# Kernel tuning notes

Measured on AMD Instinct MI355X. Metric: run time of the kernel, lower is better.

The kernel has to match this reference:

```python
import jax, jax.numpy as jnp
import numpy as np

BS, N, F, G, H, L, HFC, C, E = 8, 15135, 64, 73, 256, 3, 512, 2, 242160

def setup_inputs() -> dict:
    key = jax.random.key(0)
    ks = jax.random.split(key, 16)
    s = 0.02
    return {
        "x": jax.random.normal(ks[0], (BS, N, F), jnp.float32),
        "batch": jnp.zeros((BS,), jnp.int64),
        "edge_index": jax.random.randint(ks[1], (2, E), 0, N, jnp.int64),
        "nodes_graphlets": jax.random.uniform(ks[2], (N, G), jnp.float32),
        "W1": jax.random.normal(ks[3], (F + G, H), jnp.float32) * s,
        "b1": jnp.zeros((H,), jnp.float32),
        "W2": jax.random.normal(ks[4], (H, H), jnp.float32) * s,
        "b2": jnp.zeros((H,), jnp.float32),
        "W3": jax.random.normal(ks[5], (H, H), jnp.float32) * s,
        "b3": jnp.zeros((H,), jnp.float32),
        "fc_W": jax.random.normal(ks[6], (L * H, 1), jnp.float32) * s,
        "fc_b": jnp.zeros((1,), jnp.float32),
        "lin1_W": jax.random.normal(ks[7], (N, HFC), jnp.float32) * s,
        "lin1_b": jnp.zeros((HFC,), jnp.float32),
        "lin2_W": jax.random.normal(ks[8], (HFC, C), jnp.float32) * s,
        "lin2_b": jnp.zeros((C,), jnp.float32),
    }


def reference(x, batch, edge_index, nodes_graphlets, W1, b1, W2, b2, W3, b3,
              fc_W, fc_b, lin1_W, lin1_b, lin2_W, lin2_b):
    bs, n, _ = x.shape
    row, col = edge_index[0], edge_index[1]
    # GCN normalization with self-loops (edge_weight = 1): D^-1/2 (A+I) D^-1/2
    deg = jnp.zeros((n,), x.dtype).at[col].add(1.0) + 1.0
    dis = jax.lax.rsqrt(deg)
    norm = dis[row] * dis[col]          # [E]
    deg_inv = 1.0 / deg                 # self-loop coefficient dis[i]^2

    def gcn_conv(h, W, b):
        hw = h @ W                                  # [bs, n, H]
        msg = hw[:, row, :] * norm[None, :, None]   # gather src, scale
        agg = jnp.zeros_like(hw).at[:, col, :].add(msg)
        agg = agg + hw * deg_inv[None, :, None]     # self loops
        return agg + b

    # graphlet_mode == 'input': concat graphlet features to node features
    pe = jnp.broadcast_to(nodes_graphlets[None], (bs,) + nodes_graphlets.shape)
    h = jnp.concatenate([x, pe], axis=2)            # [bs, n, F+G]

    h1 = jax.nn.elu(gcn_conv(h, W1, b1))
    h2 = jax.nn.elu(gcn_conv(h1, W2, b2))
    h3 = jax.nn.elu(gcn_conv(h2, W3, b3))

    # mode == 'cat': stack along new last dim then flatten (torch stack+view order)
    hc = jnp.stack([h1, h2, h3], axis=-1).reshape(bs, n, -1)  # [bs, n, H*L]
    g = (hc @ fc_W + fc_b).reshape(bs, n)                     # [bs, n_genes]

    z = jax.nn.elu(g @ lin1_W + lin1_b)   # dropout: eval mode -> identity
    out = z @ lin2_W + lin2_b
    return jax.nn.log_softmax(out, axis=-1)
```

## Files before the change

kernel.cpp:

```cpp
#include <hip/hip_runtime.h>
#include <hip/hip_bf16.h>

using bf16 = __hip_bfloat16;
typedef short s16x8 __attribute__((ext_vector_type(8)));
typedef short s16x4 __attribute__((ext_vector_type(4)));
typedef float f32x4 __attribute__((ext_vector_type(4)));
typedef float f32x2 __attribute__((ext_vector_type(2)));

#define BSZ   8
#define NN    15135
#define FF    64
#define GG    73
#define HH    256
#define EE    242160
#define K1P   160
#define MREAL (BSZ * NN)
#define MPAD  (946 * 128)
#define HFC   512
#define NCHUNK 64
#define NCHUNKS ((NN + NCHUNK - 1) / NCHUNK)
#define SCANB  ((NN + 255) / 256)
#define FP8_INV_SCALE 0.015625f

#define GLOAD_LDS16(gp, lp)                                                     \
    __builtin_amdgcn_global_load_lds(                                           \
        (const __attribute__((address_space(1))) void*)(gp),                    \
        (__attribute__((address_space(3))) void*)(lp), 16, 0, 0)

__device__ __forceinline__ int colmap(int p) {
    return (p & 192) | ((p & 3) << 4) | ((p >> 2) & 15);
}

__global__ void k_deg(const int* __restrict__ col, int* __restrict__ cnt, int e) {
    int i = blockIdx.x * blockDim.x + threadIdx.x;
    if (i < e) atomicAdd(&cnt[col[i]], 1);
}

__global__ __launch_bounds__(256)
void k_scanA(const int* __restrict__ cnt, int* __restrict__ cursor,
             int* __restrict__ bsum) {
    __shared__ int ws[4];
    int i = blockIdx.x * 256 + threadIdx.x;
    int tid = threadIdx.x, lane = tid & 63, wid = tid >> 6;
    int v = (i < NN) ? cnt[i] : 0;
    int s = v;
    #pragma unroll
    for (int off = 1; off < 64; off <<= 1) {
        int t = __shfl_up(s, off);
        if (lane >= off) s += t;
    }
    if (lane == 63) ws[wid] = s;
    __syncthreads();
    int pre = 0;
    #pragma unroll
    for (int w = 0; w < 4; ++w) pre += (w < wid) ? ws[w] : 0;
    int incl = pre + s;
    if (i < NN) cursor[i] = incl;
    if (tid == 255) bsum[blockIdx.x] = incl;
}

__global__ __launch_bounds__(64)
void k_scanB(int* __restrict__ bsum, int* __restrict__ offs) {
    int t = threadIdx.x;
    int v = (t < SCANB) ? bsum[t] : 0;
    int s = v;
    #pragma unroll
    for (int off = 1; off < 64; off <<= 1) {
        int x = __shfl_up(s, off);
        if (t >= off) s += x;
    }
    if (t < SCANB) bsum[t] = s - v;
    if (t == 63) offs[NN] = s;
}

__global__ __launch_bounds__(256)
void k_scanC(const int* __restrict__ cnt, int* __restrict__ cursor,
             const int* __restrict__ bsum, int* __restrict__ offs,
             float* __restrict__ dis, float* __restrict__ dinv) {
    int i = blockIdx.x * 256 + threadIdx.x;
    if (i >= NN) return;
    int v = cnt[i];
    int excl = cursor[i] - v + bsum[blockIdx.x];
    offs[i] = excl;
    cursor[i] = excl;
    float d = (float)(v + 1);
    dis[i]  = rsqrtf(d);
    dinv[i] = (1.0f / d) * FP8_INV_SCALE;
}

__global__ void k_csr(const int* __restrict__ row, const int* __restrict__ col,
                      int* __restrict__ cursor, const float* __restrict__ dis,
                      int2* __restrict__ cpack, int e) {
    int i = blockIdx.x * blockDim.x + threadIdx.x;
    if (i >= e) return;
    int r = row[i], c = col[i];
    int p = atomicAdd(&cursor[c], 1);
    cpack[p] = make_int2(r, __float_as_int(dis[r] * dis[c] * FP8_INV_SCALE));
}

__global__ void k_prep_h0(const float* __restrict__ x, const float* __restrict__ gl,
                          bf16* __restrict__ h0) {
    int idx = blockIdx.x * blockDim.x + threadIdx.x;
    if (idx >= MREAL * (K1P / 8)) return;
    int m = idx / (K1P / 8);
    int q = idx - m * (K1P / 8);
    int j0 = q * 8;
    int n = m % NN;
    s16x8 o;
    #pragma unroll
    for (int k = 0; k < 8; ++k) {
        int j = j0 + k;
        float val;
        if (j < FF) val = x[(size_t)m * FF + j];
        else if (j < FF + GG) val = gl[(size_t)n * GG + (j - FF)];
        else val = 0.f;
        o[k] = (short)__bfloat16_as_ushort(__float2bfloat16(val));
    }
    *(s16x8*)&h0[(size_t)m * K1P + j0] = o;
}

__global__ void k_prep_w3(const float* __restrict__ W1, const float* __restrict__ W2,
                          const float* __restrict__ W3, bf16* __restrict__ W1T,
                          bf16* __restrict__ W2T, bf16* __restrict__ W3T) {
    int idx = blockIdx.x * blockDim.x + threadIdx.x;
    if (idx < 256 * K1P) {
        int nn = idx / K1P, kk = idx - nn * K1P;
        W1T[idx] = __float2bfloat16(
            kk < FF + GG ? 64.f * W1[(size_t)kk * 256 + nn] : 0.f);
    } else if (idx < 256 * K1P + 65536) {
        int j = idx - 256 * K1P;
        int nn = j >> 8, kk = j & 255;
        W2T[j] = __float2bfloat16(64.f * W2[(size_t)colmap(kk) * 256 + nn]);
    } else if (idx < 256 * K1P + 2 * 65536) {
        int j = idx - 256 * K1P - 65536;
        int nn = j >> 8, kk = j & 255;
        W3T[j] = __float2bfloat16(64.f * W3[(size_t)colmap(kk) * 256 + nn]);
    }
}

#define BK 32
template <int K>
__global__ __launch_bounds__(256)
void k_gemm(const bf16* __restrict__ A, const bf16* __restrict__ BT,
            unsigned char* __restrict__ C) {
    __shared__ __align__(16) short As[64 * BK];
    __shared__ __align__(16) short Bs[256 * BK];
    const int tid  = threadIdx.x;
    const int bm   = blockIdx.x * 64;
    const int lane = tid & 63, wave = tid >> 6;
    const int wn   = wave * 64;
    const int fr   = lane & 15, quad = lane >> 4;
    const int r    = tid >> 2;
    const int c    = (tid & 3) * 8;

    const bf16* Ap = A  + (size_t)(bm + r) * K + c;
    const bf16* Bp = BT + (size_t)r * K + c;
    short* AsT = As + tid * 8;
    short* BsT = Bs + tid * 8;

    f32x4 acc[4][4] = {};

    for (int k0 = 0; k0 < K; k0 += BK) {
        GLOAD_LDS16(Ap + k0, AsT);
        #pragma unroll
        for (int q = 0; q < 4; ++q)
            GLOAD_LDS16(Bp + (size_t)(q * 64) * K + k0, BsT + q * 64 * BK);
        __syncthreads();
        s16x8 af[4], bfv[4];
        #pragma unroll
        for (int i = 0; i < 4; ++i)
            af[i] = *(const s16x8*)&As[(i * 16 + fr) * BK + quad * 8];
        #pragma unroll
        for (int j = 0; j < 4; ++j)
            bfv[j] = *(const s16x8*)&Bs[(wn + j * 16 + fr) * BK + quad * 8];
        #pragma unroll
        for (int i = 0; i < 4; ++i)
            #pragma unroll
            for (int j = 0; j < 4; ++j)
                acc[i][j] = __builtin_amdgcn_mfma_f32_16x16x32_bf16(
                    af[i], bfv[j], acc[i][j], 0, 0, 0);
        __syncthreads();
    }

    #pragma unroll
    for (int i = 0; i < 4; ++i) {
        int rbase = bm + i * 16 + quad * 4;
        #pragma unroll
        for (int rr = 0; rr < 4; ++rr) {
            int row = rbase + rr;
            if (row >= MREAL) continue;
            unsigned wpack = (unsigned)__builtin_amdgcn_cvt_pk_fp8_f32(
                acc[i][0][rr], acc[i][1][rr], 0, false);
            wpack = (unsigned)__builtin_amdgcn_cvt_pk_fp8_f32(
                acc[i][2][rr], acc[i][3][rr], (int)wpack, true);
            *(unsigned*)&C[(size_t)row * 256 + wn + fr * 4] = wpack;
        }
    }
}

#define AGG_GRP 512
#define AGG_STRIDE (AGG_GRP * 4)
__global__ __launch_bounds__(256)
void k_agg(const unsigned char* __restrict__ hw, bf16* __restrict__ hout,
           const int* __restrict__ offs, const int2* __restrict__ cpack,
           const float* __restrict__ dinv,
           const float* __restrict__ bias, const float* __restrict__ fcW,
           float* __restrict__ g, int writeH) {
    const int b    = blockIdx.x & 7;
    const int grp  = blockIdx.x >> 3;
    const int wid  = threadIdx.x >> 6;
    const int lane = threadIdx.x & 63;
    const int wv   = grp * 4 + wid;
    const unsigned c4 = lane * 4;

    const unsigned char* hwb = hw + (size_t)b * NN * 256;

    float bias4[4], fw4[4];
    #pragma unroll
    for (int k = 0; k < 4; ++k) {
        int cl = colmap((int)c4 + k);
        bias4[k] = bias[cl];
        fw4[k]   = fcW[3 * cl];
    }

    for (int v0 = wv; v0 < NN; v0 += AGG_STRIDE) {
        const int v   = __builtin_amdgcn_readfirstlane(v0);
        const int beg = __builtin_amdgcn_readfirstlane(offs[v]);
        const int end = __builtin_amdgcn_readfirstlane(offs[v + 1]);
        const float di = dinv[v];
        f32x2 a01, a23;
        {
            unsigned q = *(const unsigned*)(hwb + (((unsigned)v) << 8) + c4);
            f32x2 t0 = __builtin_amdgcn_cvt_pk_f32_fp8(q, false);
            f32x2 t1 = __builtin_amdgcn_cvt_pk_f32_fp8(q, true);
            f32x2 dd = {di, di};
            a01 = dd * t0;
            a23 = dd * t1;
        }

        #define EDGE1(qv, mv) {                                            \
            f32x2 t0 = __builtin_amdgcn_cvt_pk_f32_fp8((qv), false);       \
            f32x2 t1 = __builtin_amdgcn_cvt_pk_f32_fp8((qv), true);        \
            f32x2 mm = {(mv), (mv)};                                       \
            a01 += mm * t0;                                                \
            a23 += mm * t1; }

        int e = beg;
        while (e + 8 <= end) {
            int2 ep[8];
            #pragma unroll
            for (int u = 0; u < 8; ++u) ep[u] = cpack[e + u];
            unsigned q[8];
            #pragma unroll
            for (int u = 0; u < 8; ++u)
                q[u] = *(const unsigned*)(hwb + (((unsigned)ep[u].x) << 8) + c4);
            #pragma unroll
            for (int u = 0; u < 8; ++u) EDGE1(q[u], __int_as_float(ep[u].y));
            e += 8;
        }
        if (e + 4 <= end) {
            int2 ep[4];
            #pragma unroll
            for (int u = 0; u < 4; ++u) ep[u] = cpack[e + u];
            unsigned q[4];
            #pragma unroll
            for (int u = 0; u < 4; ++u)
                q[u] = *(const unsigned*)(hwb + (((unsigned)ep[u].x) << 8) + c4);
            #pragma unroll
            for (int u = 0; u < 4; ++u) EDGE1(q[u], __int_as_float(ep[u].y));
            e += 4;
        }
        if (e + 2 <= end) {
            int2 ep0 = cpack[e], ep1 = cpack[e + 1];
            unsigned q0 = *(const unsigned*)(hwb + (((unsigned)ep0.x) << 8) + c4);
            unsigned q1 = *(const unsigned*)(hwb + (((unsigned)ep1.x) << 8) + c4);
            EDGE1(q0, __int_as_float(ep0.y));
            EDGE1(q1, __int_as_float(ep1.y));
            e += 2;
        }
        if (e < end) {
            int2 ep0 = cpack[e];
            unsigned q0 = *(const unsigned*)(hwb + (((unsigned)ep0.x) << 8) + c4);
            EDGE1(q0, __int_as_float(ep0.y));
        }
        #undef EDGE1

        float acc4[4] = {a01[0], a01[1], a23[0], a23[1]};
        float p = 0.f;
        s16x4 o4;
        #pragma unroll
        for (int k = 0; k < 4; ++k) {
            float hv = acc4[k] + bias4[k];
            hv = hv > 0.f ? hv : (__expf(hv) - 1.0f);
            o4[k] = (short)__bfloat16_as_ushort(__float2bfloat16(hv));
            p += hv * fw4[k];
        }
        if (writeH)
            *(s16x4*)&hout[((size_t)b * NN + v) * 256 + c4] = o4;

        #pragma unroll
        for (int off = 32; off; off >>= 1) p += __shfl_xor(p, off);
        if (lane == 0) g[(size_t)b * NN + v] += p;
    }
}

__global__ __launch_bounds__(256)
void k_lin1(const float* __restrict__ g, const float* __restrict__ fcb,
            const float* __restrict__ W, float* __restrict__ zpart) {
    const int ny = blockIdx.x;
    const int n0 = ny * NCHUNK;
    const int cnt = min(NCHUNK, NN - n0);
    const int tid = threadIdx.x;
    __shared__ float sg[8][NCHUNK];
    float fb = fcb[0];
    for (int idx = tid; idx < 8 * NCHUNK; idx += 256) {
        int b = idx / NCHUNK, nn = idx - b * NCHUNK;
        sg[b][nn] = (nn < cnt) ? (g[(size_t)b * NN + n0 + nn] + fb) : 0.f;
    }
    __syncthreads();
    float2 acc[8] = {};
    for (int nn = 0; nn < cnt; ++nn) {
        float2 w = *(const float2*)&W[(size_t)(n0 + nn) * HFC + tid * 2];
        #pragma unroll
        for (int b = 0; b < 8; ++b) {
            float gv = sg[b][nn];
            acc[b].x += gv * w.x;
            acc[b].y += gv * w.y;
        }
    }
    #pragma unroll
    for (int b = 0; b < 8; ++b)
        *(float2*)&zpart[(size_t)ny * 4096 + b * 512 + tid * 2] = acc[b];
}

__global__ __launch_bounds__(256)
void k_lin1red(const float* __restrict__ zpart, float* __restrict__ zacc) {
    int t = blockIdx.x * 256 + threadIdx.x;
    float s = 0.f;
    for (int c = 0; c < NCHUNKS; ++c) s += zpart[(size_t)c * 4096 + t];
    zacc[t] = s;
}

__global__ __launch_bounds__(512)
void k_final(const float* __restrict__ zacc, const float* __restrict__ l1b,
             const float* __restrict__ W2, const float* __restrict__ l2b,
             float* __restrict__ out) {
    __shared__ float r0[512], r1[512];
    int t = threadIdx.x;
    for (int b = 0; b < 8; ++b) {
        float zv = zacc[b * HFC + t] + l1b[t];
        zv = zv > 0.f ? zv : (__expf(zv) - 1.0f);
        r0[t] = zv * W2[t * 2 + 0];
        r1[t] = zv * W2[t * 2 + 1];
        __syncthreads();
        for (int s = 256; s; s >>= 1) {
            if (t < s) { r0[t] += r0[t + s]; r1[t] += r1[t + s]; }
            __syncthreads();
        }
        if (t == 0) {
            float o0 = r0[0] + l2b[0], o1 = r1[0] + l2b[1];
            float m = fmaxf(o0, o1);
            float lse = m + logf(expf(o0 - m) + expf(o1 - m));
            out[b * 2 + 0] = o0 - lse;
            out[b * 2 + 1] = o1 - lse;
        }
        __syncthreads();
    }
}

extern "C" void kernel_launch(void* const* d_in, const int* in_sizes, int n_in,
                              void* d_out, int out_size, void* d_ws, size_t ws_size,
                              hipStream_t stream) {
    const float* x    = (const float*)d_in[0];
    const int*   eidx = (const int*)d_in[2];
    const float* gl   = (const float*)d_in[3];
    const float* W1   = (const float*)d_in[4];
    const float* b1   = (const float*)d_in[5];
    const float* W2   = (const float*)d_in[6];
    const float* b2   = (const float*)d_in[7];
    const float* W3   = (const float*)d_in[8];
    const float* b3   = (const float*)d_in[9];
    const float* fcW  = (const float*)d_in[10];
    const float* fcb  = (const float*)d_in[11];
    const float* l1W  = (const float*)d_in[12];
    const float* l1b  = (const float*)d_in[13];
    const float* l2W  = (const float*)d_in[14];
    const float* l2b  = (const float*)d_in[15];
    float* out = (float*)d_out;

    size_t off = 0;
    auto alloc = [&](size_t bytes) {
        void* p = (char*)d_ws + off;
        off += (bytes + 255) & ~(size_t)255;
        return p;
    };
    bf16* bufA          = (bf16*)alloc((size_t)MPAD * 256 * 2);
    unsigned char* bufC = (unsigned char*)alloc((size_t)MPAD * 256);
    bf16* W1T      = (bf16*)alloc(256 * K1P * 2);
    bf16* W2T      = (bf16*)alloc(256 * 256 * 2);
    bf16* W3T      = (bf16*)alloc(256 * 256 * 2);
    int*  deg_cnt  = (int*)alloc(NN * 4);
    int*  offs     = (int*)alloc((NN + 1) * 4);
    int*  cursor   = (int*)alloc(NN * 4);
    int*  bsum     = (int*)alloc(SCANB * 4);
    float* dis     = (float*)alloc(NN * 4);
    float* dinv    = (float*)alloc(NN * 4);
    int2* cpack    = (int2*)alloc((size_t)EE * 8);
    float* g       = (float*)alloc((size_t)BSZ * NN * 4);

    float* zpart = (float*)bufC;
    float* zacc  = (float*)(bufC + (8 << 20));

    hipMemsetAsync(deg_cnt, 0, NN * 4, stream);
    hipMemsetAsync(g, 0, (size_t)BSZ * NN * 4, stream);

    const int* erow = eidx;
    const int* ecol = eidx + EE;

    k_deg<<<(EE + 255) / 256, 256, 0, stream>>>(ecol, deg_cnt, EE);
    k_scanA<<<SCANB, 256, 0, stream>>>(deg_cnt, cursor, bsum);
    k_scanB<<<1, 64, 0, stream>>>(bsum, offs);
    k_scanC<<<SCANB, 256, 0, stream>>>(deg_cnt, cursor, bsum, offs, dis, dinv);
    k_csr<<<(EE + 255) / 256, 256, 0, stream>>>(erow, ecol, cursor, dis,
                                                cpack, EE);

    k_prep_h0<<<(MREAL * (K1P / 8) + 255) / 256, 256, 0, stream>>>(x, gl, bufA);
    k_prep_w3<<<(256 * K1P + 2 * 65536 + 255) / 256, 256, 0, stream>>>(
        W1, W2, W3, W1T, W2T, W3T);

    dim3 ggrid(MPAD / 64);
    dim3 agrid(8 * AGG_GRP);

    k_gemm<K1P><<<ggrid, 256, 0, stream>>>(bufA, W1T, bufC);
    k_agg<<<agrid, 256, 0, stream>>>(bufC, bufA, offs, cpack, dinv,
                                     b1, fcW + 0, g, 1);
    k_gemm<256><<<ggrid, 256, 0, stream>>>(bufA, W2T, bufC);
    k_agg<<<agrid, 256, 0, stream>>>(bufC, bufA, offs, cpack, dinv,
                                     b2, fcW + 1, g, 1);
    k_gemm<256><<<ggrid, 256, 0, stream>>>(bufA, W3T, bufC);
    k_agg<<<agrid, 256, 0, stream>>>(bufC, bufA, offs, cpack, dinv,
                                     b3, fcW + 2, g, 0);

    k_lin1<<<NCHUNKS, 256, 0, stream>>>(g, fcb, l1W, zpart);
    k_lin1red<<<16, 256, 0, stream>>>(zpart, zacc);
    k_final<<<1, 512, 0, stream>>>(zacc, l1b, l2W, l2b, out);
}
```

Baseline: 459.8 us.

## Fuse setup kernels with grid barrier, merge prep and final reductions

Merges the degree count, three scan stages and CSR build into one persistent kernel synchronised by an atomic grid barrier. It also folds both memsets and the weight/h0 prep into a single prep kernel, and combines the lin1 reduction with the final layer into a per-batch kernel. The aggregation edge loop is unrolled to 16 edges for more loads in flight. This cuts launch count and serial tiny kernels, at the cost of relying on all 240 blocks being co-resident for the spin barrier and higher register pressure in the aggregation kernel.

```diff
diff --git a/kernel.cpp b/kernel.cpp
--- a/kernel.cpp
+++ b/kernel.cpp
@@ -31,110 +31,141 @@
     return (p & 192) | ((p & 3) << 4) | ((p >> 2) & 15);
 }
 
-__global__ void k_deg(const int* __restrict__ col, int* __restrict__ cnt, int e) {
-    int i = blockIdx.x * blockDim.x + threadIdx.x;
-    if (i < e) atomicAdd(&cnt[col[i]], 1);
-}
-
-__global__ __launch_bounds__(256)
-void k_scanA(const int* __restrict__ cnt, int* __restrict__ cursor,
-             int* __restrict__ bsum) {
-    __shared__ int ws[4];
-    int i = blockIdx.x * 256 + threadIdx.x;
-    int tid = threadIdx.x, lane = tid & 63, wid = tid >> 6;
-    int v = (i < NN) ? cnt[i] : 0;
-    int s = v;
-    #pragma unroll
-    for (int off = 1; off < 64; off <<= 1) {
-        int t = __shfl_up(s, off);
-        if (lane >= off) s += t;
-    }
-    if (lane == 63) ws[wid] = s;
-    __syncthreads();
-    int pre = 0;
-    #pragma unroll
-    for (int w = 0; w < 4; ++w) pre += (w < wid) ? ws[w] : 0;
-    int incl = pre + s;
-    if (i < NN) cursor[i] = incl;
-    if (tid == 255) bsum[blockIdx.x] = incl;
-}
-
-__global__ __launch_bounds__(64)
-void k_scanB(int* __restrict__ bsum, int* __restrict__ offs) {
-    int t = threadIdx.x;
-    int v = (t < SCANB) ? bsum[t] : 0;
-    int s = v;
-    #pragma unroll
-    for (int off = 1; off < 64; off <<= 1) {
-        int x = __shfl_up(s, off);
-        if (t >= off) s += x;
-    }
-    if (t < SCANB) bsum[t] = s - v;
-    if (t == 63) offs[NN] = s;
-}
-
-__global__ __launch_bounds__(256)
-void k_scanC(const int* __restrict__ cnt, int* __restrict__ cursor,
-             const int* __restrict__ bsum, int* __restrict__ offs,
-             float* __restrict__ dis, float* __restrict__ dinv) {
-    int i = blockIdx.x * 256 + threadIdx.x;
-    if (i >= NN) return;
-    int v = cnt[i];
-    int excl = cursor[i] - v + bsum[blockIdx.x];
-    offs[i] = excl;
-    cursor[i] = excl;
-    float d = (float)(v + 1);
-    dis[i]  = rsqrtf(d);
-    dinv[i] = (1.0f / d) * FP8_INV_SCALE;
-}
-
-__global__ void k_csr(const int* __restrict__ row, const int* __restrict__ col,
-                      int* __restrict__ cursor, const float* __restrict__ dis,
-                      int2* __restrict__ cpack, int e) {
-    int i = blockIdx.x * blockDim.x + threadIdx.x;
-    if (i >= e) return;
-    int r = row[i], c = col[i];
-    int p = atomicAdd(&cursor[c], 1);
-    cpack[p] = make_int2(r, __float_as_int(dis[r] * dis[c] * FP8_INV_SCALE));
-}
-
-__global__ void k_prep_h0(const float* __restrict__ x, const float* __restrict__ gl,
-                          bf16* __restrict__ h0) {
+#define PREP_H0_CNT (MREAL * (K1P / 8))
+#define PREP_W1_CNT (256 * K1P)
+#define PREP_W23_CNT 65536
+#define PREP_TOT (PREP_H0_CNT + PREP_W1_CNT + 2 * PREP_W23_CNT + NN + MREAL + 64)
+__global__ void k_prep(const float* __restrict__ x, const float* __restrict__ gl,
+                       bf16* __restrict__ h0,
+                       const float* __restrict__ W1, const float* __restrict__ W2,
+                       const float* __restrict__ W3, bf16* __restrict__ W1T,
+                       bf16* __restrict__ W2T, bf16* __restrict__ W3T,
+                       int* __restrict__ cnt, float* __restrict__ g,
+                       int* __restrict__ sync) {
     int idx = blockIdx.x * blockDim.x + threadIdx.x;
-    if (idx >= MREAL * (K1P / 8)) return;
-    int m = idx / (K1P / 8);
-    int q = idx - m * (K1P / 8);
-    int j0 = q * 8;
-    int n = m % NN;
-    s16x8 o;
-    #pragma unroll
-    for (int k = 0; k < 8; ++k) {
-        int j = j0 + k;
-        float val;
-        if (j < FF) val = x[(size_t)m * FF + j];
-        else if (j < FF + GG) val = gl[(size_t)n * GG + (j - FF)];
-        else val = 0.f;
-        o[k] = (short)__bfloat16_as_ushort(__float2bfloat16(val));
-    }
-    *(s16x8*)&h0[(size_t)m * K1P + j0] = o;
-}
-
-__global__ void k_prep_w3(const float* __restrict__ W1, const float* __restrict__ W2,
-                          const float* __restrict__ W3, bf16* __restrict__ W1T,
-                          bf16* __restrict__ W2T, bf16* __restrict__ W3T) {
-    int idx = blockIdx.x * blockDim.x + threadIdx.x;
-    if (idx < 256 * K1P) {
+    if (idx < PREP_H0_CNT) {
+        int m = idx / (K1P / 8);
+        int q = idx - m * (K1P / 8);
+        int j0 = q * 8;
+        int n = m % NN;
+        s16x8 o;
+        #pragma unroll
+        for (int k = 0; k < 8; ++k) {
+            int j = j0 + k;
+            float val;
+            if (j < FF) val = x[(size_t)m * FF + j];
+            else if (j < FF + GG) val = gl[(size_t)n * GG + (j - FF)];
+            else val = 0.f;
+            o[k] = (short)__bfloat16_as_ushort(__float2bfloat16(val));
+        }
+        *(s16x8*)&h0[(size_t)m * K1P + j0] = o;
+        return;
+    }
+    idx -= PREP_H0_CNT;
+    if (idx < PREP_W1_CNT) {
         int nn = idx / K1P, kk = idx - nn * K1P;
         W1T[idx] = __float2bfloat16(
             kk < FF + GG ? 64.f * W1[(size_t)kk * 256 + nn] : 0.f);
-    } else if (idx < 256 * K1P + 65536) {
-        int j = idx - 256 * K1P;
-        int nn = j >> 8, kk = j & 255;
-        W2T[j] = __float2bfloat16(64.f * W2[(size_t)colmap(kk) * 256 + nn]);
-    } else if (idx < 256 * K1P + 2 * 65536) {
-        int j = idx - 256 * K1P - 65536;
-        int nn = j >> 8, kk = j & 255;
-        W3T[j] = __float2bfloat16(64.f * W3[(size_t)colmap(kk) * 256 + nn]);
+        return;
+    }
+    idx -= PREP_W1_CNT;
+    if (idx < PREP_W23_CNT) {
+        int nn = idx >> 8, kk = idx & 255;
+        W2T[idx] = __float2bfloat16(64.f * W2[(size_t)colmap(kk) * 256 + nn]);
+        return;
+    }
+    idx -= PREP_W23_CNT;
+    if (idx < PREP_W23_CNT) {
+        int nn = idx >> 8, kk = idx & 255;
+        W3T[idx] = __float2bfloat16(64.f * W3[(size_t)colmap(kk) * 256 + nn]);
+        return;
+    }
+    idx -= PREP_W23_CNT;
+    if (idx < NN) { cnt[idx] = 0; return; }
+    idx -= NN;
+    if (idx < MREAL) { g[idx] = 0.f; return; }
+    idx -= MREAL;
+    if (idx < 64) sync[idx] = 0;
+}
+
+#define NB_SETUP 240
+__device__ __forceinline__ void gbar(int* sync, int target) {
+    __syncthreads();
+    if (threadIdx.x == 0) {
+        __threadfence();
+        atomicAdd(sync, 1);
+        while (atomicAdd(sync, 0) < target) __builtin_amdgcn_s_sleep(8);
+        __threadfence();
+    }
+    __syncthreads();
+}
+
+__global__ __launch_bounds__(256)
+void k_setup(const int* __restrict__ erow, const int* __restrict__ ecol,
+             int* __restrict__ cnt, int* __restrict__ offs,
+             int* __restrict__ cursor, int* __restrict__ bsum,
+             float* __restrict__ dis, float* __restrict__ dinv,
+             int2* __restrict__ cpack, int* __restrict__ sync) {
+    __shared__ int ws[4];
+    const int tid = threadIdx.x, bid = blockIdx.x;
+    const int gsz = NB_SETUP * 256;
+    const int gid = bid * 256 + tid;
+
+    for (int i = gid; i < EE; i += gsz) atomicAdd(&cnt[ecol[i]], 1);
+    gbar(sync, NB_SETUP);
+
+    if (bid < SCANB) {
+        int i = bid * 256 + tid;
+        int lane = tid & 63, wid = tid >> 6;
+        int v = (i < NN) ? cnt[i] : 0;
+        int s = v;
+        #pragma unroll
+        for (int off = 1; off < 64; off <<= 1) {
+            int t = __shfl_up(s, off);
+            if (lane >= off) s += t;
+        }
+        if (lane == 63) ws[wid] = s;
+        __syncthreads();
+        int pre = 0;
+        #pragma unroll
+        for (int w = 0; w < 4; ++w) pre += (w < wid) ? ws[w] : 0;
+        int incl = pre + s;
+        if (i < NN) cursor[i] = incl;
+        if (tid == 255) bsum[bid] = incl;
+    }
+    gbar(sync, 2 * NB_SETUP);
+
+    if (bid == 0 && tid < 64) {
+        int v = (tid < SCANB) ? bsum[tid] : 0;
+        int s = v;
+        #pragma unroll
+        for (int off = 1; off < 64; off <<= 1) {
+            int xx = __shfl_up(s, off);
+            if (tid >= off) s += xx;
+        }
+        if (tid < SCANB) bsum[tid] = s - v;
+        if (tid == 63) offs[NN] = s;
+    }
+    gbar(sync, 3 * NB_SETUP);
+
+    if (bid < SCANB) {
+        int i = bid * 256 + tid;
+        if (i < NN) {
+            int v = cnt[i];
+            int excl = cursor[i] - v + bsum[bid];
+            offs[i] = excl;
+            cursor[i] = excl;
+            float d = (float)(v + 1);
+            dis[i]  = rsqrtf(d);
+            dinv[i] = (1.0f / d) * FP8_INV_SCALE;
+        }
+    }
+    gbar(sync, 4 * NB_SETUP);
+
+    for (int i = gid; i < EE; i += gsz) {
+        int r = erow[i], c = ecol[i];
+        int p = atomicAdd(&cursor[c], 1);
+        cpack[p] = make_int2(r, __float_as_int(dis[r] * dis[c] * FP8_INV_SCALE));
     }
 }
 
@@ -246,7 +277,19 @@
             a23 += mm * t1; }
 
         int e = beg;
-        while (e + 8 <= end) {
+        while (e + 16 <= end) {
+            int2 ep[16];
+            #pragma unroll
+            for (int u = 0; u < 16; ++u) ep[u] = cpack[e + u];
+            unsigned q[16];
+            #pragma unroll
+            for (int u = 0; u < 16; ++u)
+                q[u] = *(const unsigned*)(hwb + (((unsigned)ep[u].x) << 8) + c4);
+            #pragma unroll
+            for (int u = 0; u < 16; ++u) EDGE1(q[u], __int_as_float(ep[u].y));
+            e += 16;
+        }
+        if (e + 8 <= end) {
             int2 ep[8];
             #pragma unroll
             for (int u = 0; u < 8; ++u) ep[u] = cpack[e + u];
@@ -333,38 +376,29 @@
         *(float2*)&zpart[(size_t)ny * 4096 + b * 512 + tid * 2] = acc[b];
 }
 
-__global__ __launch_bounds__(256)
-void k_lin1red(const float* __restrict__ zpart, float* __restrict__ zacc) {
-    int t = blockIdx.x * 256 + threadIdx.x;
+__global__ __launch_bounds__(512)
+void k_lin2(const float* __restrict__ zpart, const float* __restrict__ l1b,
+            const float* __restrict__ W2, const float* __restrict__ l2b,
+            float* __restrict__ out) {
+    __shared__ float r0[512], r1[512];
+    const int b = blockIdx.x, t = threadIdx.x;
     float s = 0.f;
-    for (int c = 0; c < NCHUNKS; ++c) s += zpart[(size_t)c * 4096 + t];
-    zacc[t] = s;
-}
-
-__global__ __launch_bounds__(512)
-void k_final(const float* __restrict__ zacc, const float* __restrict__ l1b,
-             const float* __restrict__ W2, const float* __restrict__ l2b,
-             float* __restrict__ out) {
-    __shared__ float r0[512], r1[512];
-    int t = threadIdx.x;
-    for (int b = 0; b < 8; ++b) {
-        float zv = zacc[b * HFC + t] + l1b[t];
-        zv = zv > 0.f ? zv : (__expf(zv) - 1.0f);
-        r0[t] = zv * W2[t * 2 + 0];
-        r1[t] = zv * W2[t * 2 + 1];
+    for (int c = 0; c < NCHUNKS; ++c) s += zpart[(size_t)c * 4096 + b * 512 + t];
+    float zv = s + l1b[t];
+    zv = zv > 0.f ? zv : (__expf(zv) - 1.0f);
+    r0[t] = zv * W2[t * 2 + 0];
+    r1[t] = zv * W2[t * 2 + 1];
+    __syncthreads();
+    for (int st = 256; st; st >>= 1) {
+        if (t < st) { r0[t] += r0[t + st]; r1[t] += r1[t + st]; }
         __syncthreads();
-        for (int s = 256; s; s >>= 1) {
-            if (t < s) { r0[t] += r0[t + s]; r1[t] += r1[t + s]; }
-            __syncthreads();
-        }
-        if (t == 0) {
-            float o0 = r0[0] + l2b[0], o1 = r1[0] + l2b[1];
-            float m = fmaxf(o0, o1);
-            float lse = m + logf(expf(o0 - m) + expf(o1 - m));
-            out[b * 2 + 0] = o0 - lse;
-            out[b * 2 + 1] = o1 - lse;
-        }
-        __syncthreads();
+    }
+    if (t == 0) {
+        float o0 = r0[0] + l2b[0], o1 = r1[0] + l2b[1];
+        float m = fmaxf(o0, o1);
+        float lse = m + logf(expf(o0 - m) + expf(o1 - m));
+        out[b * 2 + 0] = o0 - lse;
+        out[b * 2 + 1] = o1 - lse;
     }
 }
 
@@ -407,26 +441,18 @@
     float* dinv    = (float*)alloc(NN * 4);
     int2* cpack    = (int2*)alloc((size_t)EE * 8);
     float* g       = (float*)alloc((size_t)BSZ * NN * 4);
+    int*  sync     = (int*)alloc(64 * 4);
 
     float* zpart = (float*)bufC;
-    float* zacc  = (float*)(bufC + (8 << 20));
-
-    hipMemsetAsync(deg_cnt, 0, NN * 4, stream);
-    hipMemsetAsync(g, 0, (size_t)BSZ * NN * 4, stream);
 
     const int* erow = eidx;
     const int* ecol = eidx + EE;
 
-    k_deg<<<(EE + 255) / 256, 256, 0, stream>>>(ecol, deg_cnt, EE);
-    k_scanA<<<SCANB, 256, 0, stream>>>(deg_cnt, cursor, bsum);
-    k_scanB<<<1, 64, 0, stream>>>(bsum, offs);
-    k_scanC<<<SCANB, 256, 0, stream>>>(deg_cnt, cursor, bsum, offs, dis, dinv);
-    k_csr<<<(EE + 255) / 256, 256, 0, stream>>>(erow, ecol, cursor, dis,
-                                                cpack, EE);
-
-    k_prep_h0<<<(MREAL * (K1P / 8) + 255) / 256, 256, 0, stream>>>(x, gl, bufA);
-    k_prep_w3<<<(256 * K1P + 2 * 65536 + 255) / 256, 256, 0, stream>>>(
-        W1, W2, W3, W1T, W2T, W3T);
+    k_prep<<<(PREP_TOT + 255) / 256, 256, 0, stream>>>(
+        x, gl, bufA, W1, W2, W3, W1T, W2T, W3T, deg_cnt, g, sync);
+
+    k_setup<<<NB_SETUP, 256, 0, stream>>>(erow, ecol, deg_cnt, offs, cursor,
+                                          bsum, dis, dinv, cpack, sync);
 
     dim3 ggrid(MPAD / 64);
     dim3 agrid(8 * AGG_GRP);
@@ -442,6 +468,5 @@
                                      b3, fcW + 2, g, 0);
 
     k_lin1<<<NCHUNKS, 256, 0, stream>>>(g, fcb, l1W, zpart);
-    k_lin1red<<<16, 256, 0, stream>>>(zpart, zacc);
-    k_final<<<1, 512, 0, stream>>>(zacc, l1b, l2W, l2b, out);
-}
+    k_lin2<<<8, 512, 0, stream>>>(zpart, l1b, l2W, l2b, out);
+}
```

Result: slower. 487.4 us (+6.0%).
